# Kernel tuning notes

Measured on AMD Instinct MI355X. Metric: run time of the kernel, lower is better.

The kernel has to match this reference:

```python
import jax, jax.numpy as jnp
import numpy as np

# pywt bior2.2 decomposition filters (symmetric mode, single-level dwt)
DEC_LO = np.array([0.0, -0.1767766952966369, 0.3535533905932738,
                   1.0606601717798212, 0.3535533905932738, -0.1767766952966369],
                  dtype=np.float32)
DEC_HI = np.array([0.0, 0.3535533905932738, -0.7071067811865476,
                   0.3535533905932738, 0.0, 0.0], dtype=np.float32)


def setup_inputs() -> dict:
    key = jax.random.key(0)
    x = jax.random.normal(key, (32, 64, 16384), dtype=jnp.float32)
    return {"x": x}


def _dwt1d(x):
    """Single-level DWT matching pywt.dwt(sig, 'bior2.2', mode='symmetric').
    x: [B, C, N] -> (a, d) each [B, C, L] with L = (N + F - 1) // 2.
    pywt computes true convolution with the extended signal and keeps odd
    phases; equivalently: symmetric-pad by F-1, drop first sample, then
    stride-2 correlation with the flipped filters.
    """
    B, C, N = x.shape
    F = DEC_LO.shape[0]  # 6
    ext = jnp.pad(x, ((0, 0), (0, 0), (F - 1, F - 1)), mode='symmetric')
    ext = ext[:, :, 1:]  # odd-phase downsampling offset (pywt convention)
    inp = ext.reshape(B * C, 1, -1)  # [B*C, 1, N+2F-3]
    kern = jnp.stack([jnp.asarray(DEC_LO)[::-1],
                      jnp.asarray(DEC_HI)[::-1]])[:, None, :]  # [2, 1, F]
    y = jax.lax.conv_general_dilated(inp, kern, window_strides=(2,),
                                     padding='VALID')  # [B*C, 2, L]
    y = y.reshape(B, C, 2, -1)
    return y[:, :, 0], y[:, :, 1]


def _interp_linear(x, L):
    """torch F.interpolate(mode='linear', align_corners=False) on last dim."""
    N = x.shape[-1]
    src = (jnp.arange(L, dtype=x.dtype) + 0.5) * (N / L) - 0.5
    src = jnp.clip(src, 0.0, N - 1)
    i0 = jnp.floor(src).astype(jnp.int32)
    i1 = jnp.minimum(i0 + 1, N - 1)
    w = (src - i0).astype(x.dtype)
    return x[..., i0] * (1.0 - w) + x[..., i1] * w


def reference(x):
    a, d = _dwt1d(x)                      # [B, C, L] each
    ds = _interp_linear(x, a.shape[-1])   # [B, C, L]
    return jnp.concatenate([ds, a, d], axis=1)  # [B, 3C, L]
```

## Files before the change

### kernel.cpp

```cpp
#include <hip/hip_runtime.h>


namespace {
constexpr int kN = 16384;
constexpr int kL = 8194;
constexpr int kTPB = 256;
constexpr int kOutPerThread = 8;
constexpr int kTile = kTPB * kOutPerThread;
constexpr int kStage = 2 * kTile + 8;

__device__ __forceinline__ int symi(int j) {
    j = (j < 0) ? (-j - 1) : j;
    j = (j >= kN) ? (2 * kN - 1 - j) : j;
    return j;
}

__global__ __launch_bounds__(256) void dwt1d_kernel(const float* __restrict__ x,
                                                    float* __restrict__ out) {
    __shared__ float s[kStage];

    const int tile = blockIdx.x;
    const int row  = blockIdx.y;
    const int tid  = threadIdx.x;
    const int k0   = tile * kTile;
    const int s0   = 2 * k0 - 8;
    const int lastk = min(kL - 1, k0 + kTile - 1);
    const int cnt  = 2 * lastk - s0 + 1;
    const int nchunk = (cnt + 3) >> 2;

    const float* __restrict__ xr = x + (size_t)row * kN;

    for (int cck = tid; cck < nchunk; cck += kTPB) {
        const int g = s0 + 4 * cck;
        float4 v;
        if (g >= 0 && g + 3 < kN) {
            v = *(const float4*)(xr + g);
        } else {
            v.x = xr[symi(g)];
            v.y = xr[symi(g + 1)];
            v.z = xr[symi(g + 2)];
            v.w = xr[symi(g + 3)];
        }
        *(float4*)(s + 4 * cck) = v;
    }
    __syncthreads();

    const float LO1 = -0.1767766952966369f;
    const float LO2 = 0.3535533905932738f;
    const float LO3 = 1.0606601717798212f;
    const float HI1 = 0.3535533905932738f;
    const float HI2 = -0.7071067811865476f;
    const float scale = 16384.0f / 8194.0f;

    const int b = row >> 6;
    const int c = row & 63;
    float* __restrict__ o0 = out + ((size_t)(b * 192 + c)) * kL;
    float* __restrict__ o1 = o0 + (size_t)64 * kL;
    float* __restrict__ o2 = o0 + (size_t)128 * kL;

#pragma unroll
    for (int j = 0; j < kOutPerThread; ++j) {
        const int kk = k0 + j * kTPB + tid;
        if (kk >= kL) continue;
        const int m = 2 * (kk - k0) + 8;

        const float2 q0 = *(const float2*)(s + m - 4);
        const float2 q1 = *(const float2*)(s + m - 2);
        const float v4 = s[m];
        const float a = LO3 * q1.x + LO2 * (q0.y + q1.y) + LO1 * (q0.x + v4);
        const float d = HI2 * q1.y + HI1 * (q1.x + v4);

        float src = (kk + 0.5f) * scale - 0.5f;
        src = fminf(fmaxf(src, 0.0f), (float)(kN - 1));
        const int i0 = (int)floorf(src);
        const int i1 = min(i0 + 1, kN - 1);
        const float w = src - (float)i0;
        const float ds = s[i0 - s0] * (1.0f - w) + s[i1 - s0] * w;

        o0[kk] = ds;
        o1[kk] = a;
        o2[kk] = d;
    }
}
}

extern "C" void kernel_launch(void* const* d_in, const int* in_sizes, int n_in,
                              void* d_out, int out_size, void* d_ws, size_t ws_size,
                              hipStream_t stream) {
    const float* x = (const float*)d_in[0];
    float* out = (float*)d_out;
    dim3 grid((kL + kTile - 1) / kTile, 32 * 64);
    dwt1d_kernel<<<grid, dim3(kTPB), 0, stream>>>(x, out);
}
```

Baseline: 295.4 us.

## Replace shared-memory staging with per-thread register windows and vector stores

Drops the shared-memory tile and its barrier. Each thread now loads an 8-float window with two float4 loads and computes two outputs of each band (interp, approx, detail), written with float2 stores. The two tail outputs past N/2 are computed serially by one thread. Neighbouring windows overlap, so some reads repeat and rely on cache, but the change removes LDS traffic and synchronization and spreads the work over more blocks.

```diff
diff --git a/kernel.cpp b/kernel.cpp
--- a/kernel.cpp
+++ b/kernel.cpp
@@ -4,46 +4,29 @@
 namespace {
 constexpr int kN = 16384;
 constexpr int kL = 8194;
-constexpr int kTPB = 256;
-constexpr int kOutPerThread = 8;
-constexpr int kTile = kTPB * kOutPerThread;
-constexpr int kStage = 2 * kTile + 8;
 
 __device__ __forceinline__ int symi(int j) {
     j = (j < 0) ? (-j - 1) : j;
-    j = (j >= kN) ? (2 * kN - 1 - j) : j;
-    return j;
+    return (j >= kN) ? (2 * kN - 1 - j) : j;
 }
 
 __global__ __launch_bounds__(256) void dwt1d_kernel(const float* __restrict__ x,
                                                     float* __restrict__ out) {
-    __shared__ float s[kStage];
+    const int p = blockIdx.x * 256 + threadIdx.x;
+    const int row = blockIdx.y;
+    const float* __restrict__ xr = x + (size_t)row * kN;
+    const int w0 = 4 * p - 4;
 
-    const int tile = blockIdx.x;
-    const int row  = blockIdx.y;
-    const int tid  = threadIdx.x;
-    const int k0   = tile * kTile;
-    const int s0   = 2 * k0 - 8;
-    const int lastk = min(kL - 1, k0 + kTile - 1);
-    const int cnt  = 2 * lastk - s0 + 1;
-    const int nchunk = (cnt + 3) >> 2;
-
-    const float* __restrict__ xr = x + (size_t)row * kN;
-
-    for (int cck = tid; cck < nchunk; cck += kTPB) {
-        const int g = s0 + 4 * cck;
-        float4 v;
-        if (g >= 0 && g + 3 < kN) {
-            v = *(const float4*)(xr + g);
-        } else {
-            v.x = xr[symi(g)];
-            v.y = xr[symi(g + 1)];
-            v.z = xr[symi(g + 2)];
-            v.w = xr[symi(g + 3)];
-        }
-        *(float4*)(s + 4 * cck) = v;
+    float v[8];
+    if (p != 0) {
+        const float4 A = *(const float4*)(xr + w0);
+        const float4 B = *(const float4*)(xr + w0 + 4);
+        v[0] = A.x; v[1] = A.y; v[2] = A.z; v[3] = A.w;
+        v[4] = B.x; v[5] = B.y; v[6] = B.z; v[7] = B.w;
+    } else {
+#pragma unroll
+        for (int i = 0; i < 8; ++i) v[i] = xr[symi(w0 + i)];
     }
-    __syncthreads();
 
     const float LO1 = -0.1767766952966369f;
     const float LO2 = 0.3535533905932738f;
@@ -52,34 +35,57 @@
     const float HI2 = -0.7071067811865476f;
     const float scale = 16384.0f / 8194.0f;
 
+    float av[2], dv[2], sv[2];
+#pragma unroll
+    for (int j = 0; j < 2; ++j) {
+        av[j] = LO3 * v[2 * j + 2] + LO2 * (v[2 * j + 1] + v[2 * j + 3]) +
+                LO1 * (v[2 * j] + v[2 * j + 4]);
+        dv[j] = HI2 * v[2 * j + 3] + HI1 * (v[2 * j + 2] + v[2 * j + 4]);
+
+        const int k = 2 * p + j;
+        float src = ((float)k + 0.5f) * scale - 0.5f;
+        src = fminf(fmaxf(src, 0.0f), (float)(kN - 1));
+        const int i0 = (int)floorf(src);
+        const float w = src - (float)i0;
+        const int t = i0 - w0 - 2 * j;
+        const float x0 = (t == 0) ? v[2 * j]     : (t == 1) ? v[2 * j + 1]
+                       : (t == 2) ? v[2 * j + 2] : (t == 3) ? v[2 * j + 3]
+                                                            : v[2 * j + 4];
+        const float x1 = (t == 0) ? v[2 * j + 1] : (t == 1) ? v[2 * j + 2]
+                       : (t == 2) ? v[2 * j + 3] : (t == 3) ? v[2 * j + 4]
+                                                            : v[2 * j + 5];
+        sv[j] = x0 * (1.0f - w) + x1 * w;
+    }
+
     const int b = row >> 6;
     const int c = row & 63;
     float* __restrict__ o0 = out + ((size_t)(b * 192 + c)) * kL;
     float* __restrict__ o1 = o0 + (size_t)64 * kL;
     float* __restrict__ o2 = o0 + (size_t)128 * kL;
 
+    *(float2*)(o0 + 2 * p) = make_float2(sv[0], sv[1]);
+    *(float2*)(o1 + 2 * p) = make_float2(av[0], av[1]);
+    *(float2*)(o2 + 2 * p) = make_float2(dv[0], dv[1]);
+
+    if (p == 4095) {
 #pragma unroll
-    for (int j = 0; j < kOutPerThread; ++j) {
-        const int kk = k0 + j * kTPB + tid;
-        if (kk >= kL) continue;
-        const int m = 2 * (kk - k0) + 8;
-
-        const float2 q0 = *(const float2*)(s + m - 4);
-        const float2 q1 = *(const float2*)(s + m - 2);
-        const float v4 = s[m];
-        const float a = LO3 * q1.x + LO2 * (q0.y + q1.y) + LO1 * (q0.x + v4);
-        const float d = HI2 * q1.y + HI1 * (q1.x + v4);
-
-        float src = (kk + 0.5f) * scale - 0.5f;
-        src = fminf(fmaxf(src, 0.0f), (float)(kN - 1));
-        const int i0 = (int)floorf(src);
-        const int i1 = min(i0 + 1, kN - 1);
-        const float w = src - (float)i0;
-        const float ds = s[i0 - s0] * (1.0f - w) + s[i1 - s0] * w;
-
-        o0[kk] = ds;
-        o1[kk] = a;
-        o2[kk] = d;
+        for (int kk = kN / 2; kk < kL; ++kk) {
+            const float t0 = xr[symi(2 * kk - 4)];
+            const float t1 = xr[symi(2 * kk - 3)];
+            const float t2 = xr[symi(2 * kk - 2)];
+            const float t3 = xr[symi(2 * kk - 1)];
+            const float t4 = xr[symi(2 * kk)];
+            const float a = LO3 * t2 + LO2 * (t1 + t3) + LO1 * (t0 + t4);
+            const float d = HI2 * t3 + HI1 * (t2 + t4);
+            float src = ((float)kk + 0.5f) * scale - 0.5f;
+            src = fminf(fmaxf(src, 0.0f), (float)(kN - 1));
+            const int i0 = (int)floorf(src);
+            const int i1 = min(i0 + 1, kN - 1);
+            const float w = src - (float)i0;
+            o0[kk] = xr[i0] * (1.0f - w) + xr[i1] * w;
+            o1[kk] = a;
+            o2[kk] = d;
+        }
     }
 }
 }
@@ -89,6 +95,6 @@
                               hipStream_t stream) {
     const float* x = (const float*)d_in[0];
     float* out = (float*)d_out;
-    dim3 grid((kL + kTile - 1) / kTile, 32 * 64);
-    dwt1d_kernel<<<grid, dim3(kTPB), 0, stream>>>(x, out);
+    dim3 grid(16, 32 * 64);
+    dwt1d_kernel<<<grid, dim3(256), 0, stream>>>(x, out);
 }
```

New measurement: 301.3 us. +2.0%, slower.
